# Kernel tuning notes

Measured on AMD Instinct MI355X. Metric: run time of the kernel, lower is better.

Reference implementation:

```python
import jax, jax.numpy as jnp
import numpy as np


def _segsum(v, idx, n):
    return jax.ops.segment_sum(v, idx, num_segments=n)


def _rdl(z, n_dst, Wna, We, Wi, es, ed, is_, id_):
    """Relationship_Decoupled_layer: node softmax attn + per-edge attn.
    e-channel (mode etype): softmax over 2 logits; i-channel: sigmoid(1 logit)."""
    zd = z[:n_dst]
    node_alpha = jax.nn.softmax(zd @ Wna, axis=1)                      # [nd,2]
    e_e = jax.nn.softmax(jnp.concatenate([z[es], zd[ed]], axis=-1) @ We, axis=1)  # [Ee,2]
    e_i = jax.nn.sigmoid(jnp.concatenate([z[is_], zd[id_]], axis=-1) @ Wi)        # [Ei,1]
    return node_alpha, e_e, e_i


def _one_agg(z, n_dst, W, b, na, e_e, es, ed):
    """One_Neighbor_Aggregation: mean over nbrs of e[:,0]*Linear(z_src), relu, + alpha0*z_dst.
    Linear is applied on src nodes once (linearity) instead of per-edge."""
    zd = na[:, 0:1] * z[:n_dst]
    wz = z @ W + b                                                     # [n_src,D]
    s = _segsum(e_e[:, 0:1] * wz[es], ed, n_dst)                       # [nd,D]
    deg = _segsum(jnp.ones((es.shape[0], 1), z.dtype), ed, n_dst)
    f = jax.nn.relu(s / jnp.maximum(deg, 1.0))
    return f + zd


def _nia(z, n_dst, na, e_e, es, ed, e_i, is_, id_):
    """Neighbor_Interaction_Aggregation: e_h (mode etype, attn col 1) and i_h
    (other etype, sigmoid attn), cross term via polarization identity, + alpha1*z_dst."""
    zd = na[:, 1:2] * z[:n_dst]
    e_h = _segsum(e_e[:, 1:2] * z[es], ed, n_dst)
    i_h = _segsum(e_i * z[is_], id_, n_dst)
    inter = jax.nn.relu(0.5 * (jnp.square(e_h + i_h) - jnp.square(e_h) - jnp.square(i_h)))
    return inter + zd


def setup_inputs() -> dict:
    key = jax.random.key(0)
    ks = jax.random.split(key, 32)
    F, D, O = 256, 128, 64
    n_src0, n_dst0, E0 = 100000, 25000, 500000
    n_src1, n_dst1, E1 = 25000, 5000, 100000

    def ri(k, n, hi):
        return jax.random.randint(k, (n,), 0, hi, dtype=jnp.int32)

    inp = {
        'feat': jax.random.normal(ks[0], (n_src0, F), jnp.float32),
        'src0_cor': ri(ks[1], E0, n_src0), 'dst0_cor': ri(ks[2], E0, n_dst0),
        'src0_sim': ri(ks[3], E0, n_src0), 'dst0_sim': ri(ks[4], E0, n_dst0),
        'src1_cor': ri(ks[5], E1, n_src1), 'dst1_cor': ri(ks[6], E1, n_dst1),
        'src1_sim': ri(ks[7], E1, n_src1), 'dst1_sim': ri(ks[8], E1, n_dst1),
        'n_dst0': n_dst0, 'n_dst1': n_dst1,
    }
    s = 0.05  # keep attention logits / activations in a sane range
    inp['Win'] = jax.random.normal(ks[9], (2, F, D)) * s
    inp['b_in'] = jnp.zeros((2, D), jnp.float32)
    inp['na1'] = jax.random.normal(ks[10], (2, D, 2)) * s
    inp['ea1'] = jax.random.normal(ks[11], (2, 2 * D, 2)) * s
    inp['ia1'] = jax.random.normal(ks[12], (2, 2 * D, 1)) * s
    inp['W1'] = jax.random.normal(ks[13], (2, D, D)) * s
    inp['b1'] = jnp.zeros((2, D), jnp.float32)
    inp['na2'] = jax.random.normal(ks[14], (2, D, 2)) * s
    inp['ea2'] = jax.random.normal(ks[15], (2, 2 * D, 2)) * s
    inp['ia2'] = jax.random.normal(ks[16], (2, 2 * D, 1)) * s
    inp['W2'] = jax.random.normal(ks[17], (2, D, D)) * s
    inp['b2'] = jnp.zeros((2, D), jnp.float32)
    inp['Wout'] = jax.random.normal(ks[18], (2, D, O)) * s
    inp['bout'] = jnp.zeros((2, O), jnp.float32)
    return inp


def reference(feat, src0_cor, dst0_cor, src0_sim, dst0_sim,
              src1_cor, dst1_cor, src1_sim, dst1_sim, n_dst0, n_dst1,
              Win, b_in, na1, ea1, ia1, W1, b1, na2, ea2, ia2, W2, b2, Wout, bout):
    # mode index 0 = 'cor', 1 = 'sim'; e-channel = mode etype, i-channel = other etype
    blk0 = {0: (src0_cor, dst0_cor, src0_sim, dst0_sim),
            1: (src0_sim, dst0_sim, src0_cor, dst0_cor)}
    blk1 = {0: (src1_cor, dst1_cor, src1_sim, dst1_sim),
            1: (src1_sim, dst1_sim, src1_cor, dst1_cor)}
    outs = []
    for m in range(2):
        es0, ed0, is0, id0 = blk0[m]
        es1, ed1, is1, id1 = blk1[m]
        z = feat @ Win[m] + b_in[m]                                    # fc_input (eval: dropout = identity)
        # layer 1 on block0
        na, ee, ei = _rdl(z, n_dst0, na1[m], ea1[m], ia1[m], es0, ed0, is0, id0)
        one = _one_agg(z, n_dst0, W1[m], b1[m], na, ee, es0, ed0)
        nia = _nia(z, n_dst0, na, ee, es0, ed0, ei, is0, id0)
        z = 0.5 * (one + nia)                                          # [n_dst0, D]
        # layer 2 on block1
        na, ee, ei = _rdl(z, n_dst1, na2[m], ea2[m], ia2[m], es1, ed1, is1, id1)
        one = _one_agg(z, n_dst1, W2[m], b2[m], na, ee, es1, ed1)
        nia = _nia(z, n_dst1, na, ee, es1, ed1, ei, is1, id1)
        z = 0.5 * (one + nia)                                          # [n_dst1, D]
        outs.append(z @ Wout[m] + bout[m])
    return jnp.stack(outs)                                             # [2, n_dst1, O] (cor, sim)
```

## Files before the change

### kernel.cpp

```cpp
#include <hip/hip_runtime.h>
#include <hip/hip_bf16.h>
#include <math.h>

#define F_DIM 256
#define D_DIM 128
#define O_DIM 64
#define NS0   100000
#define ND0   25000
#define E0_N  500000
#define NS1   25000
#define ND1   5000
#define E1_N  100000

#define NBE0  1954
#define NBE1  391
#define NB_CSR (2 * NBE0 + 2 * NBE1)
#define NB_WPREP 576

typedef __attribute__((ext_vector_type(8))) short s8v;
typedef __attribute__((ext_vector_type(4))) float f4v;

struct CPtr4 { const int *p0, *p1, *p2, *p3; };
struct MPtr4 { int *p0, *p1, *p2, *p3; };

__device__ __forceinline__ float2 unpack2(uint u) {
    union { uint i; float f; } a, b;
    a.i = (u & 0xffffu) << 16; b.i = u & 0xffff0000u;
    return make_float2(a.f, b.f);
}
__device__ __forceinline__ ushort f2bf(float f) {
    __hip_bfloat16 h = __float2bfloat16(f);
    return *(ushort*)&h;
}
__device__ __forceinline__ float u2f(uint u) {
    union { uint i; float f; } v; v.i = u; return v.f;
}
__device__ __forceinline__ uint f2u(float f) {
    union { uint i; float f; } v; v.f = f; return v.i;
}

__global__ __launch_bounds__(256) void gemm_l0(
    const float* __restrict__ A,
    const ushort* __restrict__ Btb,
    const float* __restrict__ biasb,
    ushort* __restrict__ Coutb, size_t coutstr, int M)
{
    constexpr int PA = 40;
    __shared__ ushort As[64 * PA];
    __shared__ ushort Bs[2][128 * PA];

    const int tid = threadIdx.x;
    const int row0 = blockIdx.x * 64;
    const int wave = tid >> 6, lane = tid & 63;
    const int l15 = lane & 15, l4 = lane >> 4;
    const int wm0 = (wave >> 1) * 32;
    const int wn0 = (wave & 1) * 64;

    f4v acc[2][2][4];
    #pragma unroll
    for (int m2 = 0; m2 < 2; ++m2)
        #pragma unroll
        for (int i = 0; i < 2; ++i)
            #pragma unroll
            for (int j = 0; j < 4; ++j)
                acc[m2][i][j] = (f4v)(0.0f);

    for (int kc = 0; kc < F_DIM; kc += 32) {
        __syncthreads();
        {
            int r = tid >> 2, g = (tid & 3) * 8;
            int gr = row0 + r;
            float4 v0 = make_float4(0.f, 0.f, 0.f, 0.f);
            float4 v1 = make_float4(0.f, 0.f, 0.f, 0.f);
            if (gr < M) {
                v0 = *(const float4*)(A + (size_t)gr * F_DIM + kc + g);
                v1 = *(const float4*)(A + (size_t)gr * F_DIM + kc + g + 4);
            }
            ushort4 o0, o1;
            o0.x = f2bf(v0.x); o0.y = f2bf(v0.y); o0.z = f2bf(v0.z); o0.w = f2bf(v0.w);
            o1.x = f2bf(v1.x); o1.y = f2bf(v1.y); o1.z = f2bf(v1.z); o1.w = f2bf(v1.w);
            *(ushort4*)(&As[r * PA + g]) = o0;
            *(ushort4*)(&As[r * PA + g + 4]) = o1;
        }
        #pragma unroll
        for (int m2 = 0; m2 < 2; ++m2)
            #pragma unroll
            for (int it = 0; it < 2; ++it) {
                int f = tid + it * 256;
                int r = f >> 2, g = (f & 3) * 8;
                *(float4*)(&Bs[m2][r * PA + g]) =
                    *(const float4*)(Btb + m2 * (D_DIM * F_DIM) + (size_t)r * F_DIM + kc + g);
            }
        __syncthreads();

        s8v af[2];
        #pragma unroll
        for (int i = 0; i < 2; ++i)
            af[i] = *(const s8v*)(&As[(wm0 + i * 16 + l15) * PA + l4 * 8]);
        #pragma unroll
        for (int m2 = 0; m2 < 2; ++m2) {
            s8v bfr[4];
            #pragma unroll
            for (int j = 0; j < 4; ++j)
                bfr[j] = *(const s8v*)(&Bs[m2][(wn0 + j * 16 + l15) * PA + l4 * 8]);
            #pragma unroll
            for (int i = 0; i < 2; ++i)
                #pragma unroll
                for (int j = 0; j < 4; ++j)
                    acc[m2][i][j] = __builtin_amdgcn_mfma_f32_16x16x32_bf16(
                        af[i], bfr[j], acc[m2][i][j], 0, 0, 0);
        }
    }

    #pragma unroll
    for (int m2 = 0; m2 < 2; ++m2)
        #pragma unroll
        for (int i = 0; i < 2; ++i)
            #pragma unroll
            for (int ii = 0; ii < 4; ++ii) {
                int row = row0 + wm0 + i * 16 + l4 * 4 + ii;
                if (row < M) {
                    #pragma unroll
                    for (int j = 0; j < 4; ++j) {
                        int col = wn0 + j * 16 + l15;
                        Coutb[m2 * coutstr + (size_t)row * D_DIM + col] =
                            f2bf(acc[m2][i][j][ii] + biasb[m2 * D_DIM + col]);
                    }
                }
            }
}

template<int NW, int KD, int EPI>
__global__ __launch_bounds__(256) void mfma_gemm(
    const ushort* __restrict__ Ab, size_t astr,
    const ushort* __restrict__ Btb, size_t btstr,
    const float* __restrict__ biasb, size_t bstr,
    const float* __restrict__ cvecb, size_t cvstr,
    const float* __restrict__ partialb, size_t pstr,
    void* __restrict__ Coutb, size_t coutstr, int M)
{
    const int m = blockIdx.y;
    const ushort* A = Ab + m * astr;
    const ushort* Bt = Btb + m * btstr;
    const float* bias = biasb + m * bstr;
    const float* cvec = (EPI == 2) ? cvecb + m * cvstr : nullptr;
    const float* partial = (EPI == 2) ? partialb + m * pstr : nullptr;
    char* Cout = (char*)Coutb + m * coutstr * (EPI == 1 ? 4 : 2);

    constexpr int PA = 40;
    constexpr int WAVES_M = (NW == 128) ? 2 : 4;
    constexpr int WM = 128 / WAVES_M;
    constexpr int TM = WM / 16;
    constexpr int TN = 4;
    __shared__ ushort As[128 * PA];
    __shared__ ushort Bs[NW * PA];

    const int tid  = threadIdx.x;
    const int row0 = blockIdx.x * 128;
    const int wave = tid >> 6, lane = tid & 63;
    const int l15 = lane & 15, l4 = lane >> 4;
    int wm0, wn0;
    if (NW == 128) { wm0 = (wave >> 1) * 64; wn0 = (wave & 1) * 64; }
    else           { wm0 = wave * WM;        wn0 = 0; }

    f4v acc[TM][TN];
    #pragma unroll
    for (int i = 0; i < TM; ++i)
        #pragma unroll
        for (int j = 0; j < TN; ++j)
            acc[i][j] = (f4v)(0.0f);

    for (int kc = 0; kc < KD; kc += 32) {
        __syncthreads();
        #pragma unroll
        for (int it = 0; it < 2; ++it) {
            int f = tid + it * 256;
            int r = f >> 2, g = (f & 3) * 8;
            int gr = row0 + r;
            float4 v = make_float4(0.f, 0.f, 0.f, 0.f);
            if (gr < M) v = *(const float4*)(A + (size_t)gr * KD + kc + g);
            *(float4*)(&As[r * PA + g]) = v;
        }
        #pragma unroll
        for (int it = 0; it < NW * 32 / (256 * 8); ++it) {
            int f = tid + it * 256;
            int r = f >> 2, g = (f & 3) * 8;
            *(float4*)(&Bs[r * PA + g]) = *(const float4*)(Bt + (size_t)r * KD + kc + g);
        }
        __syncthreads();

        s8v af[TM], bfr[TN];
        #pragma unroll
        for (int i = 0; i < TM; ++i)
            af[i] = *(const s8v*)(&As[(wm0 + i * 16 + l15) * PA + l4 * 8]);
        #pragma unroll
        for (int j = 0; j < TN; ++j)
            bfr[j] = *(const s8v*)(&Bs[(wn0 + j * 16 + l15) * PA + l4 * 8]);
        #pragma unroll
        for (int i = 0; i < TM; ++i)
            #pragma unroll
            for (int j = 0; j < TN; ++j)
                acc[i][j] = __builtin_amdgcn_mfma_f32_16x16x32_bf16(
                    af[i], bfr[j], acc[i][j], 0, 0, 0);
    }

    #pragma unroll
    for (int i = 0; i < TM; ++i) {
        #pragma unroll
        for (int ii = 0; ii < 4; ++ii) {
            int row = row0 + wm0 + i * 16 + l4 * 4 + ii;
            if (row < M) {
                #pragma unroll
                for (int j = 0; j < TN; ++j) {
                    int col = wn0 + j * 16 + l15;
                    float a = acc[i][j][ii];
                    if (EPI == 1) {
                        ((float*)Cout)[(size_t)row * NW + col] = a + bias[col];
                    } else {
                        float val = a + cvec[row] * bias[col];
                        float o = partial[(size_t)row * NW + col] + 0.5f * fmaxf(val, 0.f);
                        ((ushort*)Cout)[(size_t)row * NW + col] = f2bf(o);
                    }
                }
            }
        }
    }
}

__global__ void histo4_prep(CPtr4 ed, MPtr4 cnt,
    const float* __restrict__ Win, const float* __restrict__ W1,
    const float* __restrict__ W2,  const float* __restrict__ Wout,
    ushort* __restrict__ Wtin, ushort* __restrict__ Wt1,
    ushort* __restrict__ Wt2,  ushort* __restrict__ Wtout)
{
    int b = blockIdx.x, t = threadIdx.x;
    if (b >= NB_CSR) {
        int i = (b - NB_CSR) * 256 + t;
        if (i < 65536) {
            int m = i >> 15, r = i & 32767, k = r >> 7, n = r & 127;
            Wtin[m * 32768 + n * 256 + k] = f2bf(Win[m * 32768 + k * 128 + n]);
        } else if (i < 98304) {
            int i2 = i - 65536;
            int m = i2 >> 14, r = i2 & 16383, k = r >> 7, n = r & 127;
            Wt1[m * 16384 + n * 128 + k] = f2bf(W1[m * 16384 + k * 128 + n]);
        } else if (i < 131072) {
            int i2 = i - 98304;
            int m = i2 >> 14, r = i2 & 16383, k = r >> 7, n = r & 127;
            Wt2[m * 16384 + n * 128 + k] = f2bf(W2[m * 16384 + k * 128 + n]);
        } else if (i < 147456) {
            int i2 = i - 131072;
            int m = i2 >> 13, r = i2 & 8191, k = r >> 6, n = r & 63;
            Wtout[m * 8192 + n * 128 + k] = f2bf(Wout[m * 8192 + k * 64 + n]);
        }
        return;
    }
    const int* edp; int* cp; int e, E;
    if (b < NBE0)          { edp = ed.p0; cp = cnt.p0; e = b * 256 + t;              E = E0_N; }
    else if (b < 2 * NBE0) { edp = ed.p1; cp = cnt.p1; e = (b - NBE0) * 256 + t;     E = E0_N; }
    else if (b < 2 * NBE0 + NBE1)
                           { edp = ed.p2; cp = cnt.p2; e = (b - 2 * NBE0) * 256 + t; E = E1_N; }
    else                   { edp = ed.p3; cp = cnt.p3; e = (b - 2 * NBE0 - NBE1) * 256 + t; E = E1_N; }
    if (e < E) atomicAdd(&cp[edp[e]], 1);
}

__global__ __launch_bounds__(1024) void exscan4(MPtr4 cnt, MPtr4 row, MPtr4 head)
{
    __shared__ int part[1024];
    const int b = blockIdx.x, t = threadIdx.x;
    int* cp; int* rp; int* hp; int n;
    if (b == 0)      { cp = cnt.p0; rp = row.p0; hp = head.p0; n = ND0; }
    else if (b == 1) { cp = cnt.p1; rp = row.p1; hp = head.p1; n = ND0; }
    else if (b == 2) { cp = cnt.p2; rp = row.p2; hp = head.p2; n = ND1; }
    else             { cp = cnt.p3; rp = row.p3; hp = head.p3; n = ND1; }

    const int chunk = (n + 1023) >> 10;
    const int start = t * chunk;
    int s = 0;
    for (int i = 0; i < chunk; ++i) {
        int idx = start + i;
        if (idx < n) s += cp[idx];
    }
    part[t] = s;
    __syncthreads();
    for (int off = 1; off < 1024; off <<= 1) {
        int v = (t >= off) ? part[t - off] : 0;
        __syncthreads();
        part[t] += v;
        __syncthreads();
    }
    int run = (t == 0) ? 0 : part[t - 1];
    for (int i = 0; i < chunk; ++i) {
        int idx = start + i;
        if (idx < n) { rp[idx] = run; hp[idx] = run; run += cp[idx]; }
    }
    if (t == 1023) rp[n] = part[1023];
}

__global__ void build4(CPtr4 es, CPtr4 ed, MPtr4 head, MPtr4 src)
{
    int b = blockIdx.x, t = threadIdx.x;
    const int *esp, *edp; int *hp, *sp; int e, E;
    if (b < NBE0)          { esp = es.p0; edp = ed.p0; hp = head.p0; sp = src.p0; e = b * 256 + t;              E = E0_N; }
    else if (b < 2 * NBE0) { esp = es.p1; edp = ed.p1; hp = head.p1; sp = src.p1; e = (b - NBE0) * 256 + t;     E = E0_N; }
    else if (b < 2 * NBE0 + NBE1)
                           { esp = es.p2; edp = ed.p2; hp = head.p2; sp = src.p2; e = (b - 2 * NBE0) * 256 + t; E = E1_N; }
    else                   { esp = es.p3; edp = ed.p3; hp = head.p3; sp = src.p3; e = (b - 2 * NBE0 - NBE1) * 256 + t; E = E1_N; }
    if (e >= E) return;
    int p = atomicAdd(&hp[edp[e]], 1);
    sp[p] = esp[e];
}

#define NP_NPB 128
__global__ __launch_bounds__(256) void node_proj(
    const ushort* __restrict__ zb, size_t zstr,
    const float* __restrict__ Web, const float* __restrict__ Wib,
    float* __restrict__ psb, float* __restrict__ qsb,
    float* __restrict__ pdb, float* __restrict__ qdb,
    int n_src, int n_dst)
{
    const int m = blockIdx.y;
    const ushort* z = zb + m * zstr;
    const float* We = Web + m * 512;
    const float* Wi = Wib + m * 256;
    float* ps = psb + (size_t)m * NS0 * 2;
    float* qs = qsb + (size_t)m * NS0;
    float* pd = pdb + (size_t)m * ND0 * 2;
    float* qd = qdb + (size_t)m * ND0;

    __shared__ float w[6][D_DIM];
    for (int k = threadIdx.x; k < D_DIM; k += 256) {
        w[0][k] = We[k * 2 + 0];
        w[1][k] = We[k * 2 + 1];
        w[2][k] = Wi[k];
        w[3][k] = We[(D_DIM + k) * 2 + 0];
        w[4][k] = We[(D_DIM + k) * 2 + 1];
        w[5][k] = Wi[D_DIM + k];
    }
    __syncthreads();

    const int sub = threadIdx.x & 7;
    const int g   = threadIdx.x >> 3;

    float wr[6][16];
    #pragma unroll
    for (int c = 0; c < 6; ++c)
        #pragma unroll
        for (int q = 0; q < 4; ++q) {
            float4 f = *(const float4*)(&w[c][sub * 16 + q * 4]);
            wr[c][q * 4 + 0] = f.x; wr[c][q * 4 + 1] = f.y;
            wr[c][q * 4 + 2] = f.z; wr[c][q * 4 + 3] = f.w;
        }

    #pragma unroll
    for (int it = 0; it < 4; ++it) {
        int node = blockIdx.x * NP_NPB + it * 32 + g;
        if (node >= n_src) continue;
        const ushort* zp = z + (size_t)node * D_DIM + sub * 16;
        uint4 ra = *(const uint4*)zp;
        uint4 rb = *(const uint4*)(zp + 8);
        uint rr[8] = {ra.x, ra.y, ra.z, ra.w, rb.x, rb.y, rb.z, rb.w};
        float p[6] = {0.f, 0.f, 0.f, 0.f, 0.f, 0.f};
        #pragma unroll
        for (int e = 0; e < 8; ++e) {
            float2 f2 = unpack2(rr[e]);
            #pragma unroll
            for (int c = 0; c < 6; ++c)
                p[c] += f2.x * wr[c][2 * e] + f2.y * wr[c][2 * e + 1];
        }
        #pragma unroll
        for (int off = 4; off > 0; off >>= 1)
            #pragma unroll
            for (int c = 0; c < 6; ++c)
                p[c] += __shfl_down(p[c], off);

        if (sub == 0) {
            *(float2*)(ps + (size_t)node * 2) = make_float2(p[0], p[1]);
            qs[node] = p[2];
            if (node < n_dst) {
                *(float2*)(pd + (size_t)node * 2) = make_float2(p[3], p[4]);
                qd[node] = p[5];
            }
        }
    }
}

__global__ __launch_bounds__(256) void edge_gather(
    const ushort* __restrict__ zb, size_t zstr,
    const float* __restrict__ psb, const float* __restrict__ pdb,
    const float* __restrict__ qsb, const float* __restrict__ qdb,
    const int* __restrict__ row_c, const int* __restrict__ src_c,
    const int* __restrict__ row_s, const int* __restrict__ src_s,
    ushort* __restrict__ h0base, float* __restrict__ partialb,
    float* __restrict__ cvecb, int n_dst)
{
    __shared__ uint2 sc[4][64];

    const int m = blockIdx.y;
    const int wv = threadIdx.x >> 6;
    const int d = blockIdx.x * 4 + wv;
    const int lane = threadIdx.x & 63;
    if (d >= n_dst) return;

    const ushort* z = zb + m * zstr;
    const float* ps = psb + (size_t)m * NS0 * 2;
    const float* qs = qsb + (size_t)m * NS0;
    const float* pdv = pdb + (size_t)m * ND0 * 2;
    const float* qdv = qdb + (size_t)m * ND0;
    const int* erow = m ? row_s : row_c;
    const int* esrc = m ? src_s : src_c;
    const int* irow = m ? row_c : row_s;
    const int* isrc = m ? src_c : src_s;
    ushort* h0b = h0base + (size_t)m * ND0 * D_DIM;
    float* partial = partialb + (size_t)m * ND0 * D_DIM;
    float* cvec = cvecb + (size_t)m * ND0;

    const float pd0 = pdv[2 * d], pd1 = pdv[2 * d + 1];
    const float qdd = qdv[d];

    float h0x = 0.f, h0y = 0.f, szx = 0.f, szy = 0.f;
    float ihx = 0.f, ihy = 0.f;
    float se0 = 0.f;

    const int b0 = erow[d], b1 = erow[d + 1];
    for (int base = b0; base < b1; base += 64) {
        const int cnt = min(64, b1 - base);
        if (lane < cnt) {
            int s = esrc[base + lane];
            float2 pp = *(const float2*)(ps + 2 * (size_t)s);
            float l0 = pp.x + pd0, l1 = pp.y + pd1;
            float mx = fmaxf(l0, l1);
            float x0 = __expf(l0 - mx), x1 = __expf(l1 - mx);
            float e0 = x0 / (x0 + x1);
            sc[wv][lane] = make_uint2(f2u(e0), (uint)s);
            se0 += e0;
        }
        asm volatile("s_waitcnt lgkmcnt(0)" ::: "memory");
        const int kf = cnt & ~7;
        int k = 0;
        for (; k < kf; k += 8) {
            uint2 ew[8]; uint rr[8];
            #pragma unroll
            for (int t = 0; t < 8; ++t) ew[t] = sc[wv][k + t];
            #pragma unroll
            for (int t = 0; t < 8; ++t) rr[t] = *(const uint*)(z + (size_t)ew[t].y * D_DIM + lane * 2);
            #pragma unroll
            for (int t = 0; t < 8; ++t) {
                float w0 = u2f(ew[t].x);
                float2 v = unpack2(rr[t]);
                szx += v.x; szy += v.y;
                h0x += w0 * v.x; h0y += w0 * v.y;
            }
        }
        if (k < cnt) {
            uint2 ew[8]; uint rr[8];
            #pragma unroll
            for (int t = 0; t < 8; ++t) ew[t] = sc[wv][(k + t) & 63];
            #pragma unroll
            for (int t = 0; t < 8; ++t) {
                uint s = (k + t < cnt) ? ew[t].y : 0u;
                rr[t] = *(const uint*)(z + (size_t)s * D_DIM + lane * 2);
            }
            #pragma unroll
            for (int t = 0; t < 8; ++t) {
                float sel = (k + t < cnt) ? 1.0f : 0.0f;
                float w0 = u2f(ew[t].x) * sel;
                float2 v = unpack2(rr[t]);
                szx += v.x * sel; szy += v.y * sel;
                h0x += w0 * v.x; h0y += w0 * v.y;
            }
        }
    }

    #pragma unroll
    for (int off = 32; off > 0; off >>= 1)
        se0 += __shfl_down(se0, off);
    if (lane == 0) cvec[d] = se0 / fmaxf((float)(b1 - b0), 1.0f);

    const int c0 = irow[d], c1 = irow[d + 1];
    for (int base = c0; base < c1; base += 64) {
        const int cnt = min(64, c1 - base);
        if (lane < cnt) {
            int s = isrc[base + lane];
            float q = qs[s] + qdd;
            float sg = 1.0f / (1.0f + __expf(-q));
            sc[wv][lane] = make_uint2(f2u(sg), (uint)s);
        }
        asm volatile("s_waitcnt lgkmcnt(0)" ::: "memory");
        const int kf = cnt & ~7;
        int k = 0;
        for (; k < kf; k += 8) {
            uint2 ew[8]; uint rr[8];
            #pragma unroll
            for (int t = 0; t < 8; ++t) ew[t] = sc[wv][k + t];
            #pragma unroll
            for (int t = 0; t < 8; ++t) rr[t] = *(const uint*)(z + (size_t)ew[t].y * D_DIM + lane * 2);
            #pragma unroll
            for (int t = 0; t < 8; ++t) {
                float g = u2f(ew[t].x);
                float2 v = unpack2(rr[t]);
                ihx += g * v.x; ihy += g * v.y;
            }
        }
        if (k < cnt) {
            uint2 ew[8]; uint rr[8];
            #pragma unroll
            for (int t = 0; t < 8; ++t) ew[t] = sc[wv][(k + t) & 63];
            #pragma unroll
            for (int t = 0; t < 8; ++t) {
                uint s = (k + t < cnt) ? ew[t].y : 0u;
                rr[t] = *(const uint*)(z + (size_t)s * D_DIM + lane * 2);
            }
            #pragma unroll
            for (int t = 0; t < 8; ++t) {
                float sel = (k + t < cnt) ? 1.0f : 0.0f;
                float g = u2f(ew[t].x) * sel;
                float2 v = unpack2(rr[t]);
                ihx += g * v.x; ihy += g * v.y;
            }
        }
    }

    float ehx = szx - h0x, ehy = szy - h0y;
    float inv = 1.0f / fmaxf((float)(b1 - b0), 1.0f);
    uint hp = (uint)f2bf(h0x * inv) | ((uint)f2bf(h0y * inv) << 16);
    *(uint*)(h0b + (size_t)d * D_DIM + lane * 2) = hp;

    float2 zd = unpack2(*(const uint*)(z + (size_t)d * D_DIM + lane * 2));
    float px = 0.5f * (fmaxf(ehx * ihx, 0.f) + zd.x);
    float py = 0.5f * (fmaxf(ehy * ihy, 0.f) + zd.y);
    *(float2*)(partial + (size_t)d * D_DIM + lane * 2) = make_float2(px, py);
}

extern "C" void kernel_launch(void* const* d_in, const int* in_sizes, int n_in,
                              void* d_out, int out_size, void* d_ws, size_t ws_size,
                              hipStream_t stream)
{
    const float* feat = (const float*)d_in[0];
    const int* src0_cor = (const int*)d_in[1];
    const int* dst0_cor = (const int*)d_in[2];
    const int* src0_sim = (const int*)d_in[3];
    const int* dst0_sim = (const int*)d_in[4];
    const int* src1_cor = (const int*)d_in[5];
    const int* dst1_cor = (const int*)d_in[6];
    const int* src1_sim = (const int*)d_in[7];
    const int* dst1_sim = (const int*)d_in[8];
    const float* Win  = (const float*)d_in[11];
    const float* b_in = (const float*)d_in[12];
    const float* ea1  = (const float*)d_in[14];
    const float* ia1  = (const float*)d_in[15];
    const float* W1   = (const float*)d_in[16];
    const float* b1   = (const float*)d_in[17];
    const float* ea2  = (const float*)d_in[19];
    const float* ia2  = (const float*)d_in[20];
    const float* W2   = (const float*)d_in[21];
    const float* b2   = (const float*)d_in[22];
    const float* Wout = (const float*)d_in[23];
    const float* bout = (const float*)d_in[24];
    (void)in_sizes; (void)n_in; (void)out_size; (void)ws_size;

    char* wsb = (char*)d_ws;
    size_t off = 0;
    auto alloc_f = [&](size_t n) { float*  p = (float*) (wsb + off); off += n * 4; return p; };
    auto alloc_i = [&](size_t n) { int*    p = (int*)   (wsb + off); off += n * 4; return p; };
    auto alloc_h = [&](size_t n) { ushort* p = (ushort*)(wsb + off); off += ((n * 2 + 15) & ~15ull); return p; };

    ushort* z0b   = alloc_h((size_t)2 * NS0 * D_DIM);
    ushort* z1b   = alloc_h((size_t)2 * NS1 * D_DIM);
    ushort* z2b   = alloc_h((size_t)2 * ND1 * D_DIM);
    ushort* h0b   = alloc_h((size_t)2 * ND0 * D_DIM);
    ushort* Wtin  = alloc_h((size_t)2 * D_DIM * F_DIM);
    ushort* Wt1   = alloc_h((size_t)2 * D_DIM * D_DIM);
    ushort* Wt2   = alloc_h((size_t)2 * D_DIM * D_DIM);
    ushort* Wtout = alloc_h((size_t)2 * O_DIM * D_DIM);

    float* ps      = alloc_f((size_t)2 * NS0 * 2);
    float* qs      = alloc_f((size_t)2 * NS0);
    float* pd      = alloc_f((size_t)2 * ND0 * 2);
    float* qd      = alloc_f((size_t)2 * ND0);
    float* cvec    = alloc_f((size_t)2 * ND0);
    float* partial = alloc_f((size_t)2 * ND0 * D_DIM);

    int* src_c0 = alloc_i(E0_N); int* row_c0 = alloc_i(ND0 + 1);
    int* src_s0 = alloc_i(E0_N); int* row_s0 = alloc_i(ND0 + 1);
    int* src_c1 = alloc_i(E1_N); int* row_c1 = alloc_i(ND1 + 1);
    int* src_s1 = alloc_i(E1_N); int* row_s1 = alloc_i(ND1 + 1);
    int* cnt_all  = alloc_i(2 * ND0 + 2 * ND1);
    int* head_all = alloc_i(2 * ND0 + 2 * ND1);

    int* cnt_c0 = cnt_all;            int* head_c0 = head_all;
    int* cnt_s0 = cnt_all + ND0;      int* head_s0 = head_all + ND0;
    int* cnt_c1 = cnt_all + 2 * ND0;  int* head_c1 = head_all + 2 * ND0;
    int* cnt_s1 = cnt_c1 + ND1;       int* head_s1 = head_c1 + ND1;

    hipMemsetAsync(cnt_all, 0, (size_t)(2 * ND0 + 2 * ND1) * 4, stream);
    {
        CPtr4 edp  = {dst0_cor, dst0_sim, dst1_cor, dst1_sim};
        CPtr4 esp  = {src0_cor, src0_sim, src1_cor, src1_sim};
        MPtr4 cntp = {cnt_c0, cnt_s0, cnt_c1, cnt_s1};
        MPtr4 rowp = {row_c0, row_s0, row_c1, row_s1};
        MPtr4 hdp  = {head_c0, head_s0, head_c1, head_s1};
        MPtr4 srcp = {src_c0, src_s0, src_c1, src_s1};
        histo4_prep<<<NB_CSR + NB_WPREP, 256, 0, stream>>>(
            edp, cntp, Win, W1, W2, Wout, Wtin, Wt1, Wt2, Wtout);
        exscan4<<<4, 1024, 0, stream>>>(cntp, rowp, hdp);
        build4<<<NB_CSR, 256, 0, stream>>>(esp, edp, hdp, srcp);
    }

    const size_t Z0S = (size_t)NS0 * D_DIM, Z1S = (size_t)NS1 * D_DIM;
    const size_t Z2S = (size_t)ND1 * D_DIM, H0S = (size_t)ND0 * D_DIM;

    gemm_l0<<<(NS0 + 63) / 64, 256, 0, stream>>>(
        feat, Wtin, b_in, z0b, Z0S, NS0);

    node_proj<<<dim3((NS0 + NP_NPB - 1) / NP_NPB, 2), 256, 0, stream>>>(
        z0b, Z0S, ea1, ia1, ps, qs, pd, qd, NS0, ND0);
    edge_gather<<<dim3((ND0 + 3) / 4, 2), 256, 0, stream>>>(
        z0b, Z0S, ps, pd, qs, qd, row_c0, src_c0, row_s0, src_s0,
        h0b, partial, cvec, ND0);
    mfma_gemm<128, 128, 2><<<dim3((ND0 + 127) / 128, 2), 256, 0, stream>>>(
        h0b, H0S, Wt1, (size_t)D_DIM * D_DIM, b1, D_DIM,
        cvec, ND0, partial, H0S, z1b, Z1S, ND0);

    node_proj<<<dim3((NS1 + NP_NPB - 1) / NP_NPB, 2), 256, 0, stream>>>(
        z1b, Z1S, ea2, ia2, ps, qs, pd, qd, NS1, ND1);
    edge_gather<<<dim3((ND1 + 3) / 4, 2), 256, 0, stream>>>(
        z1b, Z1S, ps, pd, qs, qd, row_c1, src_c1, row_s1, src_s1,
        h0b, partial, cvec, ND1);
    mfma_gemm<128, 128, 2><<<dim3((ND1 + 127) / 128, 2), 256, 0, stream>>>(
        h0b, H0S, Wt2, (size_t)D_DIM * D_DIM, b2, D_DIM,
        cvec, ND0, partial, H0S, z2b, Z2S, ND1);

    mfma_gemm<64, 128, 1><<<dim3((ND1 + 127) / 128, 2), 256, 0, stream>>>(
        z2b, Z2S, Wtout, (size_t)O_DIM * D_DIM, bout, O_DIM,
        nullptr, 0, nullptr, 0, (float*)d_out, (size_t)ND1 * O_DIM, ND1);
}
```

Baseline: 549.6 us.

## Fuse layer-0 node projection into input GEMM and interleave per-node logits

The first-layer node projection (edge/interaction logits per node) is now computed inside the input GEMM epilogue from an LDS-staged bf16 tile, which removes a separate kernel that re-read the whole 100k x 128 z tensor. Per-node source logits for both metapaths are packed into float4 records (ecor/esim) so that the edge gather fetches one aligned 16-byte record per source. The GEMM's shared memory is repurposed as a 32KB pool, and the epilogue adds weight loads, shuffles and a barrier to every GEMM block.

After: 565.1 us. 2.8% more time.

```diff
diff --git a/kernel.cpp b/kernel.cpp
--- a/kernel.cpp
+++ b/kernel.cpp
@@ -43,11 +43,17 @@
     const float* __restrict__ A,
     const ushort* __restrict__ Btb,
     const float* __restrict__ biasb,
-    ushort* __restrict__ Coutb, size_t coutstr, int M)
+    const float* __restrict__ Web,
+    const float* __restrict__ Wib,
+    ushort* __restrict__ Coutb, size_t coutstr,
+    float4* __restrict__ ecor, float4* __restrict__ esim,
+    float* __restrict__ pdb, float* __restrict__ qdb,
+    int M, int n_dst)
 {
     constexpr int PA = 40;
-    __shared__ ushort As[64 * PA];
-    __shared__ ushort Bs[2][128 * PA];
+    __shared__ __align__(16) char pool[32768];
+    ushort* As = (ushort*)pool;
+    ushort* Bsb = (ushort*)(pool + 64 * PA * 2);
 
     const int tid = threadIdx.x;
     const int row0 = blockIdx.x * 64;
@@ -88,7 +94,7 @@
             for (int it = 0; it < 2; ++it) {
                 int f = tid + it * 256;
                 int r = f >> 2, g = (f & 3) * 8;
-                *(float4*)(&Bs[m2][r * PA + g]) =
+                *(float4*)(&Bsb[m2 * 128 * PA + r * PA + g]) =
                     *(const float4*)(Btb + m2 * (D_DIM * F_DIM) + (size_t)r * F_DIM + kc + g);
             }
         __syncthreads();
@@ -102,7 +108,7 @@
             s8v bfr[4];
             #pragma unroll
             for (int j = 0; j < 4; ++j)
-                bfr[j] = *(const s8v*)(&Bs[m2][(wn0 + j * 16 + l15) * PA + l4 * 8]);
+                bfr[j] = *(const s8v*)(&Bsb[m2 * 128 * PA + (wn0 + j * 16 + l15) * PA + l4 * 8]);
             #pragma unroll
             for (int i = 0; i < 2; ++i)
                 #pragma unroll
@@ -112,22 +118,86 @@
         }
     }
 
+    __syncthreads();
+    ushort* zs = (ushort*)pool;
     #pragma unroll
     for (int m2 = 0; m2 < 2; ++m2)
         #pragma unroll
         for (int i = 0; i < 2; ++i)
             #pragma unroll
             for (int ii = 0; ii < 4; ++ii) {
-                int row = row0 + wm0 + i * 16 + l4 * 4 + ii;
+                int r = wm0 + i * 16 + l4 * 4 + ii;
+                int row = row0 + r;
                 if (row < M) {
                     #pragma unroll
                     for (int j = 0; j < 4; ++j) {
                         int col = wn0 + j * 16 + l15;
-                        Coutb[m2 * coutstr + (size_t)row * D_DIM + col] =
-                            f2bf(acc[m2][i][j][ii] + biasb[m2 * D_DIM + col]);
+                        ushort u = f2bf(acc[m2][i][j][ii] + biasb[m2 * D_DIM + col]);
+                        Coutb[m2 * coutstr + (size_t)row * D_DIM + col] = u;
+                        zs[m2 * 8192 + r * 128 + col] = u;
                     }
                 }
             }
+    __syncthreads();
+
+    {
+        const int m2 = tid >> 7;
+        const int sub = tid & 7;
+        const int gg = (tid >> 3) & 15;
+        const float* We = Web + m2 * 512;
+        const float* Wi = Wib + m2 * 256;
+
+        float wr[6][16];
+        #pragma unroll
+        for (int kk = 0; kk < 16; ++kk) {
+            int k = sub * 16 + kk;
+            wr[0][kk] = We[k * 2 + 0];
+            wr[1][kk] = We[k * 2 + 1];
+            wr[2][kk] = Wi[k];
+            wr[3][kk] = We[(D_DIM + k) * 2 + 0];
+            wr[4][kk] = We[(D_DIM + k) * 2 + 1];
+            wr[5][kk] = Wi[D_DIM + k];
+        }
+
+        #pragma unroll
+        for (int it = 0; it < 4; ++it) {
+            int r = it * 16 + gg;
+            int node = row0 + r;
+            if (node >= M) continue;
+            const ushort* zp = zs + m2 * 8192 + r * 128 + sub * 16;
+            uint4 ra = *(const uint4*)zp;
+            uint4 rb = *(const uint4*)(zp + 8);
+            uint rr[8] = {ra.x, ra.y, ra.z, ra.w, rb.x, rb.y, rb.z, rb.w};
+            float p[6] = {0.f, 0.f, 0.f, 0.f, 0.f, 0.f};
+            #pragma unroll
+            for (int e = 0; e < 8; ++e) {
+                float2 f2 = unpack2(rr[e]);
+                #pragma unroll
+                for (int c = 0; c < 6; ++c)
+                    p[c] += f2.x * wr[c][2 * e] + f2.y * wr[c][2 * e + 1];
+            }
+            #pragma unroll
+            for (int off = 4; off > 0; off >>= 1)
+                #pragma unroll
+                for (int c = 0; c < 6; ++c)
+                    p[c] += __shfl_down(p[c], off);
+
+            if (sub == 0) {
+                if (m2 == 0) {
+                    *(float2*)&ecor[node] = make_float2(p[0], p[1]);
+                    ((float*)&esim[node])[2] = p[2];
+                } else {
+                    *(float2*)&esim[node] = make_float2(p[0], p[1]);
+                    ((float*)&ecor[node])[2] = p[2];
+                }
+                if (node < n_dst) {
+                    *(float2*)(pdb + (size_t)m2 * ND0 * 2 + 2 * (size_t)node) =
+                        make_float2(p[3], p[4]);
+                    qdb[(size_t)m2 * ND0 + node] = p[5];
+                }
+            }
+        }
+    }
 }
 
 template<int NW, int KD, int EPI>
@@ -314,7 +384,7 @@
 __global__ __launch_bounds__(256) void node_proj(
     const ushort* __restrict__ zb, size_t zstr,
     const float* __restrict__ Web, const float* __restrict__ Wib,
-    float* __restrict__ psb, float* __restrict__ qsb,
+    float4* __restrict__ ecor, float4* __restrict__ esim,
     float* __restrict__ pdb, float* __restrict__ qdb,
     int n_src, int n_dst)
 {
@@ -322,10 +392,6 @@
     const ushort* z = zb + m * zstr;
     const float* We = Web + m * 512;
     const float* Wi = Wib + m * 256;
-    float* ps = psb + (size_t)m * NS0 * 2;
-    float* qs = qsb + (size_t)m * NS0;
-    float* pd = pdb + (size_t)m * ND0 * 2;
-    float* qd = qdb + (size_t)m * ND0;
 
     __shared__ float w[6][D_DIM];
     for (int k = threadIdx.x; k < D_DIM; k += 256) {
@@ -374,20 +440,25 @@
                 p[c] += __shfl_down(p[c], off);
 
         if (sub == 0) {
-            *(float2*)(ps + (size_t)node * 2) = make_float2(p[0], p[1]);
-            qs[node] = p[2];
+            if (m == 0) {
+                *(float2*)&ecor[node] = make_float2(p[0], p[1]);
+                ((float*)&esim[node])[2] = p[2];
+            } else {
+                *(float2*)&esim[node] = make_float2(p[0], p[1]);
+                ((float*)&ecor[node])[2] = p[2];
+            }
             if (node < n_dst) {
-                *(float2*)(pd + (size_t)node * 2) = make_float2(p[3], p[4]);
-                qd[node] = p[5];
-            }
-        }
-    }
-}
-
-__global__ __launch_bounds__(256) void edge_gather(
+                *(float2*)(pdb + (size_t)m * ND0 * 2 + 2 * (size_t)node) = make_float2(p[3], p[4]);
+                qdb[(size_t)m * ND0 + node] = p[5];
+            }
+        }
+    }
+}
+
+__global__ __launch_bounds__(256) void edge_gather4(
     const ushort* __restrict__ zb, size_t zstr,
-    const float* __restrict__ psb, const float* __restrict__ pdb,
-    const float* __restrict__ qsb, const float* __restrict__ qdb,
+    const float4* __restrict__ ecor, const float4* __restrict__ esim,
+    const float* __restrict__ pdb, const float* __restrict__ qdb,
     const int* __restrict__ row_c, const int* __restrict__ src_c,
     const int* __restrict__ row_s, const int* __restrict__ src_s,
     ushort* __restrict__ h0base, float* __restrict__ partialb,
@@ -401,21 +472,19 @@
     const int lane = threadIdx.x & 63;
     if (d >= n_dst) return;
 
-    const ushort* z = zb + m * zstr;
-    const float* ps = psb + (size_t)m * NS0 * 2;
-    const float* qs = qsb + (size_t)m * NS0;
-    const float* pdv = pdb + (size_t)m * ND0 * 2;
-    const float* qdv = qdb + (size_t)m * ND0;
+    const ushort* z = zb + (size_t)m * zstr;
+    const ushort* zlane = z + lane * 2;
+
     const int* erow = m ? row_s : row_c;
     const int* esrc = m ? src_s : src_c;
     const int* irow = m ? row_c : row_s;
     const int* isrc = m ? src_c : src_s;
-    ushort* h0b = h0base + (size_t)m * ND0 * D_DIM;
-    float* partial = partialb + (size_t)m * ND0 * D_DIM;
-    float* cvec = cvecb + (size_t)m * ND0;
-
-    const float pd0 = pdv[2 * d], pd1 = pdv[2 * d + 1];
-    const float qdd = qdv[d];
+    const float4* etab = m ? esim : ecor;
+    const float4* itab = m ? ecor : esim;
+
+    const float pd0 = pdb[(size_t)m * ND0 * 2 + 2 * d];
+    const float pd1 = pdb[(size_t)m * ND0 * 2 + 2 * d + 1];
+    const float qdd = qdb[(size_t)m * ND0 + d];
 
     float h0x = 0.f, h0y = 0.f, szx = 0.f, szy = 0.f;
     float ihx = 0.f, ihy = 0.f;
@@ -426,8 +495,8 @@
         const int cnt = min(64, b1 - base);
         if (lane < cnt) {
             int s = esrc[base + lane];
-            float2 pp = *(const float2*)(ps + 2 * (size_t)s);
-            float l0 = pp.x + pd0, l1 = pp.y + pd1;
+            float2 t = *(const float2*)&etab[s];
+            float l0 = t.x + pd0, l1 = t.y + pd1;
             float mx = fmaxf(l0, l1);
             float x0 = __expf(l0 - mx), x1 = __expf(l1 - mx);
             float e0 = x0 / (x0 + x1);
@@ -442,7 +511,7 @@
             #pragma unroll
             for (int t = 0; t < 8; ++t) ew[t] = sc[wv][k + t];
             #pragma unroll
-            for (int t = 0; t < 8; ++t) rr[t] = *(const uint*)(z + (size_t)ew[t].y * D_DIM + lane * 2);
+            for (int t = 0; t < 8; ++t) rr[t] = *(const uint*)(zlane + (size_t)ew[t].y * D_DIM);
             #pragma unroll
             for (int t = 0; t < 8; ++t) {
                 float w0 = u2f(ew[t].x);
@@ -458,7 +527,7 @@
             #pragma unroll
             for (int t = 0; t < 8; ++t) {
                 uint s = (k + t < cnt) ? ew[t].y : 0u;
-                rr[t] = *(const uint*)(z + (size_t)s * D_DIM + lane * 2);
+                rr[t] = *(const uint*)(zlane + (size_t)s * D_DIM);
             }
             #pragma unroll
             for (int t = 0; t < 8; ++t) {
@@ -474,15 +543,16 @@
     #pragma unroll
     for (int off = 32; off > 0; off >>= 1)
         se0 += __shfl_down(se0, off);
-    if (lane == 0) cvec[d] = se0 / fmaxf((float)(b1 - b0), 1.0f);
+    if (lane == 0)
+        cvecb[(size_t)m * ND0 + d] = se0 / fmaxf((float)(b1 - b0), 1.0f);
 
     const int c0 = irow[d], c1 = irow[d + 1];
     for (int base = c0; base < c1; base += 64) {
         const int cnt = min(64, c1 - base);
         if (lane < cnt) {
             int s = isrc[base + lane];
-            float q = qs[s] + qdd;
-            float sg = 1.0f / (1.0f + __expf(-q));
+            float ti = ((const float*)&itab[s])[2];
+            float sg = 1.0f / (1.0f + __expf(-(ti + qdd)));
             sc[wv][lane] = make_uint2(f2u(sg), (uint)s);
         }
         asm volatile("s_waitcnt lgkmcnt(0)" ::: "memory");
@@ -493,7 +563,7 @@
             #pragma unroll
             for (int t = 0; t < 8; ++t) ew[t] = sc[wv][k + t];
             #pragma unroll
-            for (int t = 0; t < 8; ++t) rr[t] = *(const uint*)(z + (size_t)ew[t].y * D_DIM + lane * 2);
+            for (int t = 0; t < 8; ++t) rr[t] = *(const uint*)(zlane + (size_t)ew[t].y * D_DIM);
             #pragma unroll
             for (int t = 0; t < 8; ++t) {
                 float g = u2f(ew[t].x);
@@ -508,7 +578,7 @@
             #pragma unroll
             for (int t = 0; t < 8; ++t) {
                 uint s = (k + t < cnt) ? ew[t].y : 0u;
-                rr[t] = *(const uint*)(z + (size_t)s * D_DIM + lane * 2);
+                rr[t] = *(const uint*)(zlane + (size_t)s * D_DIM);
             }
             #pragma unroll
             for (int t = 0; t < 8; ++t) {
@@ -520,15 +590,18 @@
         }
     }
 
+    const int nE = b1 - b0;
     float ehx = szx - h0x, ehy = szy - h0y;
-    float inv = 1.0f / fmaxf((float)(b1 - b0), 1.0f);
+    float inv = 1.0f / fmaxf((float)nE, 1.0f);
     uint hp = (uint)f2bf(h0x * inv) | ((uint)f2bf(h0y * inv) << 16);
-    *(uint*)(h0b + (size_t)d * D_DIM + lane * 2) = hp;
-
-    float2 zd = unpack2(*(const uint*)(z + (size_t)d * D_DIM + lane * 2));
+    const size_t MSTR = (size_t)ND0 * D_DIM;
+    *(uint*)(h0base + (size_t)m * MSTR + (size_t)d * D_DIM + lane * 2) = hp;
+
+    float2 zd = unpack2(*(const uint*)(zlane + (size_t)d * D_DIM));
     float px = 0.5f * (fmaxf(ehx * ihx, 0.f) + zd.x);
     float py = 0.5f * (fmaxf(ehy * ihy, 0.f) + zd.y);
-    *(float2*)(partial + (size_t)d * D_DIM + lane * 2) = make_float2(px, py);
+    *(float2*)(partialb + (size_t)m * MSTR + (size_t)d * D_DIM + lane * 2) =
+        make_float2(px, py);
 }
 
 extern "C" void kernel_launch(void* const* d_in, const int* in_sizes, int n_in,
@@ -560,9 +633,10 @@
 
     char* wsb = (char*)d_ws;
     size_t off = 0;
-    auto alloc_f = [&](size_t n) { float*  p = (float*) (wsb + off); off += n * 4; return p; };
-    auto alloc_i = [&](size_t n) { int*    p = (int*)   (wsb + off); off += n * 4; return p; };
-    auto alloc_h = [&](size_t n) { ushort* p = (ushort*)(wsb + off); off += ((n * 2 + 15) & ~15ull); return p; };
+    auto alloc_f  = [&](size_t n) { float*  p = (float*) (wsb + off); off += n * 4; return p; };
+    auto alloc_f4 = [&](size_t n) { float4* p = (float4*)(wsb + off); off += n * 16; return p; };
+    auto alloc_i  = [&](size_t n) { int*    p = (int*)   (wsb + off); off += n * 4; return p; };
+    auto alloc_h  = [&](size_t n) { ushort* p = (ushort*)(wsb + off); off += ((n * 2 + 15) & ~15ull); return p; };
 
     ushort* z0b   = alloc_h((size_t)2 * NS0 * D_DIM);
     ushort* z1b   = alloc_h((size_t)2 * NS1 * D_DIM);
@@ -573,8 +647,8 @@
     ushort* Wt2   = alloc_h((size_t)2 * D_DIM * D_DIM);
     ushort* Wtout = alloc_h((size_t)2 * O_DIM * D_DIM);
 
-    float* ps      = alloc_f((size_t)2 * NS0 * 2);
-    float* qs      = alloc_f((size_t)2 * NS0);
+    float4* ecor   = alloc_f4((size_t)NS0);
+    float4* esim   = alloc_f4((size_t)NS0);
     float* pd      = alloc_f((size_t)2 * ND0 * 2);
     float* qd      = alloc_f((size_t)2 * ND0);
     float* cvec    = alloc_f((size_t)2 * ND0);
@@ -610,21 +684,20 @@
     const size_t Z2S = (size_t)ND1 * D_DIM, H0S = (size_t)ND0 * D_DIM;
 
     gemm_l0<<<(NS0 + 63) / 64, 256, 0, stream>>>(
-        feat, Wtin, b_in, z0b, Z0S, NS0);
-
-    node_proj<<<dim3((NS0 + NP_NPB - 1) / NP_NPB, 2), 256, 0, stream>>>(
-        z0b, Z0S, ea1, ia1, ps, qs, pd, qd, NS0, ND0);
-    edge_gather<<<dim3((ND0 + 3) / 4, 2), 256, 0, stream>>>(
-        z0b, Z0S, ps, pd, qs, qd, row_c0, src_c0, row_s0, src_s0,
+        feat, Wtin, b_in, ea1, ia1, z0b, Z0S,
+        ecor, esim, pd, qd, NS0, ND0);
+
+    edge_gather4<<<dim3((ND0 + 3) / 4, 2), 256, 0, stream>>>(
+        z0b, Z0S, ecor, esim, pd, qd, row_c0, src_c0, row_s0, src_s0,
         h0b, partial, cvec, ND0);
     mfma_gemm<128, 128, 2><<<dim3((ND0 + 127) / 128, 2), 256, 0, stream>>>(
         h0b, H0S, Wt1, (size_t)D_DIM * D_DIM, b1, D_DIM,
         cvec, ND0, partial, H0S, z1b, Z1S, ND0);
 
     node_proj<<<dim3((NS1 + NP_NPB - 1) / NP_NPB, 2), 256, 0, stream>>>(
-        z1b, Z1S, ea2, ia2, ps, qs, pd, qd, NS1, ND1);
-    edge_gather<<<dim3((ND1 + 3) / 4, 2), 256, 0, stream>>>(
-        z1b, Z1S, ps, pd, qs, qd, row_c1, src_c1, row_s1, src_s1,
+        z1b, Z1S, ea2, ia2, ecor, esim, pd, qd, NS1, ND1);
+    edge_gather4<<<dim3((ND1 + 3) / 4, 2), 256, 0, stream>>>(
+        z1b, Z1S, ecor, esim, pd, qd, row_c1, src_c1, row_s1, src_s1,
         h0b, partial, cvec, ND1);
     mfma_gemm<128, 128, 2><<<dim3((ND1 + 127) / 128, 2), 256, 0, stream>>>(
         h0b, H0S, Wt2, (size_t)D_DIM * D_DIM, b2, D_DIM,
```
